# Kernel tuning notes

Hardware: AMD Instinct MI355X
Metric: run time of the kernel (lower is better)

## Reference

```python
import jax, jax.numpy as jnp
import numpy as np

D_MODEL = 2048
N_HEADS = 16
D_HEAD = 128
ROPE_BASE = 10000.0


def _rope(q, k, start_pos):
    # q, k: [B, H, S, Dh]; standard rotate-half RoPE
    S, Dh = q.shape[-2], q.shape[-1]
    inv_freq = 1.0 / (ROPE_BASE ** (jnp.arange(0, Dh, 2, dtype=jnp.float32) / Dh))  # [Dh/2]
    pos = jnp.arange(S, dtype=jnp.float32) + start_pos                              # [S]
    ang = pos[:, None] * inv_freq[None, :]                                          # [S, Dh/2]
    cos = jnp.concatenate([jnp.cos(ang), jnp.cos(ang)], axis=-1)[None, None]        # [1,1,S,Dh]
    sin = jnp.concatenate([jnp.sin(ang), jnp.sin(ang)], axis=-1)[None, None]

    def rot_half(t):
        t1, t2 = jnp.split(t, 2, axis=-1)
        return jnp.concatenate([-t2, t1], axis=-1)

    return q * cos + rot_half(q) * sin, k * cos + rot_half(k) * sin


def setup_inputs() -> dict:
    key = jax.random.key(0)
    k1, k2, k3 = jax.random.split(key, 3)
    B, S = 2, 2048
    scale_in = 1.0 / np.sqrt(D_MODEL)
    x = jax.random.normal(k1, (B, S, D_MODEL), dtype=jnp.float32)
    w_qkv = jax.random.normal(k2, (3 * D_MODEL, D_MODEL), dtype=jnp.float32) * scale_in
    w_out = jax.random.normal(k3, (D_MODEL, D_MODEL), dtype=jnp.float32) * scale_in
    return {"x": x, "w_qkv": w_qkv, "w_out": w_out, "start_pos": 0}


def reference(x, w_qkv, w_out, start_pos):
    B, S, _ = x.shape
    scale = 1.0 / np.sqrt(D_HEAD)
    qkv = jnp.einsum('bsd,ed->bse', x, w_qkv)                 # [B,S,3D]
    q, k, v = jnp.split(qkv, 3, axis=-1)
    # [B,S,D] -> [B,H,S,Dh]
    reshape = lambda t: t.reshape(B, S, N_HEADS, D_HEAD).transpose(0, 2, 1, 3)
    q, k, v = reshape(q), reshape(k), reshape(v)
    q, k = _rope(q, k, start_pos)
    scores = jnp.einsum('bhqd,bhkd->bhqk', q, k) * scale      # [B,H,S,S]
    if S > 1:
        causal = jnp.tril(jnp.ones((S, S), dtype=bool))
        scores = jnp.where(causal[None, None], scores, -jnp.inf)
    attn = jax.nn.softmax(scores, axis=-1)
    out = jnp.einsum('bhqk,bhkd->bhqd', attn, v)              # [B,H,S,Dh]
    out = out.transpose(0, 2, 1, 3).reshape(B, S, D_MODEL)
    return jnp.einsum('bsd,ed->bse', out, w_out)
```

## Files before the change

kernel.cpp:

```cpp
#include <hip/hip_runtime.h>

typedef unsigned short ushort;
typedef __attribute__((ext_vector_type(8))) short short8;
typedef __attribute__((ext_vector_type(4))) float f32x4;

#define NH 16
#define DH 128
#define SEQ 2048
#define DMODEL 2048
#define GK 2048

__device__ __forceinline__ ushort f2bf(float f) {
  union { float f; unsigned u; } v; v.f = f;
  unsigned u = v.u;
  unsigned r = (u + 0x7fffu + ((u >> 16) & 1u)) >> 16;
  return (ushort)r;
}
__device__ __forceinline__ float bf2f(ushort h) {
  union { unsigned u; float f; } v; v.u = ((unsigned)h) << 16; return v.f;
}

__device__ __forceinline__ void async16(const ushort* g, ushort* l) {
  __builtin_amdgcn_global_load_lds(
      (const __attribute__((address_space(1))) unsigned*)g,
      (__attribute__((address_space(3))) unsigned*)l, 16, 0, 0);
}

#define NX  2097152
#define NWQ 3145728
#define NWO 1048576
__global__ void cast3_kernel(const float* __restrict__ x, const float* __restrict__ wq,
                             const float* __restrict__ wo, ushort* __restrict__ xb,
                             ushort* __restrict__ wqb, ushort* __restrict__ wob) {
  int i = blockIdx.x * blockDim.x + threadIdx.x;
  int stride = gridDim.x * blockDim.x;
  for (; i < NX + NWQ + NWO; i += stride) {
    const float* s; ushort* d; int j;
    if (i < NX)            { s = x;  d = xb;  j = i; }
    else if (i < NX + NWQ) { s = wq; d = wqb; j = i - NX; }
    else                   { s = wo; d = wob; j = i - NX - NWQ; }
    float4 v = ((const float4*)s)[j];
    unsigned long long p = (unsigned long long)f2bf(v.x)
                         | ((unsigned long long)f2bf(v.y) << 16)
                         | ((unsigned long long)f2bf(v.z) << 32)
                         | ((unsigned long long)f2bf(v.w) << 48);
    ((unsigned long long*)d)[j] = p;
  }
}

template<int MODE, int NTK, int BN>
__global__ __launch_bounds__(512, 1)
void gemmk(const ushort* __restrict__ A, const ushort* __restrict__ B, int N,
           ushort* __restrict__ oq, ushort* __restrict__ ok, ushort* __restrict__ ov,
           float* __restrict__ of) {
  constexpr int NF = BN / 64;
  constexpr int WN = BN / 4;
  __shared__ ushort As[2][256 * 64];
  __shared__ ushort Bs[2][BN * 64];
  const int tid = threadIdx.x;
  const int lane = tid & 63;
  const int w = tid >> 6;
  const int wm = w >> 2, wn = w & 3;
  const int g = lane >> 4, l16 = lane & 15;
  const int m0 = blockIdx.y * 256;
  const int n0 = blockIdx.x * BN;
  const ushort* Ablk = A + (size_t)m0 * GK;
  const ushort* Bblk = B + (size_t)n0 * GK;

  const int r0 = tid >> 3, sl = tid & 7;
  const int gcol = ((sl * 16) ^ ((r0 & 7) << 4)) >> 1;
  const int ldsb = r0 * 64 + sl * 8;

  f32x4 acc[8][NF];
#pragma unroll
  for (int mf = 0; mf < 8; ++mf)
#pragma unroll
    for (int nf = 0; nf < NF; ++nf) acc[mf][nf] = (f32x4)0.f;

  short8 ra[4], rb[NF];
#pragma unroll
  for (int j = 0; j < 4; ++j)
    ra[j] = *(const short8*)(Ablk + (size_t)(j * 64 + r0) * GK + gcol);
#pragma unroll
  for (int j = 0; j < NF; ++j)
    rb[j] = *(const short8*)(Bblk + (size_t)(j * 64 + r0) * GK + gcol);
#pragma unroll
  for (int j = 0; j < 4; ++j) *(short8*)&As[0][j * 4096 + ldsb] = ra[j];
#pragma unroll
  for (int j = 0; j < NF; ++j) *(short8*)&Bs[0][j * 4096 + ldsb] = rb[j];
#pragma unroll
  for (int j = 0; j < 4; ++j)
    ra[j] = *(const short8*)(Ablk + (size_t)(j * 64 + r0) * GK + 64 + gcol);
#pragma unroll
  for (int j = 0; j < NF; ++j)
    rb[j] = *(const short8*)(Bblk + (size_t)(j * 64 + r0) * GK + 64 + gcol);
#pragma unroll
  for (int j = 0; j < 4; ++j) *(short8*)&As[1][j * 4096 + ldsb] = ra[j];
#pragma unroll
  for (int j = 0; j < NF; ++j) *(short8*)&Bs[1][j * 4096 + ldsb] = rb[j];
  __syncthreads();

  for (int t = 0; t < NTK; ++t) {
    const bool pre = (t + 2 < NTK);
    if (pre) {
      const int kt = (t + 2) * 64;
#pragma unroll
      for (int j = 0; j < 4; ++j)
        ra[j] = *(const short8*)(Ablk + (size_t)(j * 64 + r0) * GK + kt + gcol);
#pragma unroll
      for (int j = 0; j < NF; ++j)
        rb[j] = *(const short8*)(Bblk + (size_t)(j * 64 + r0) * GK + kt + gcol);
    }
    __builtin_amdgcn_sched_barrier(0);

    const ushort* cA = As[t & 1];
    const ushort* cB = Bs[t & 1];
    short8 bfr[NF][2];
#pragma unroll
    for (int nf = 0; nf < NF; ++nf) {
      int row = wn * WN + nf * 16 + l16;
#pragma unroll
      for (int ks = 0; ks < 2; ++ks)
        bfr[nf][ks] = *(const short8*)&cB[row * 64 + (((ks * 64 + g * 16) ^ ((l16 & 7) << 4)) >> 1)];
    }
#pragma unroll
    for (int p = 0; p < 4; ++p) {
      short8 af[2][2];
#pragma unroll
      for (int mi = 0; mi < 2; ++mi) {
        int row = wm * 128 + (2 * p + mi) * 16 + l16;
#pragma unroll
        for (int ks = 0; ks < 2; ++ks)
          af[mi][ks] = *(const short8*)&cA[row * 64 + (((ks * 64 + g * 16) ^ ((l16 & 7) << 4)) >> 1)];
      }
      __builtin_amdgcn_s_setprio(1);
#pragma unroll
      for (int mi = 0; mi < 2; ++mi)
#pragma unroll
        for (int nf = 0; nf < NF; ++nf)
#pragma unroll
          for (int ks = 0; ks < 2; ++ks)
            acc[2 * p + mi][nf] = __builtin_amdgcn_mfma_f32_16x16x32_bf16(
                af[mi][ks], bfr[nf][ks], acc[2 * p + mi][nf], 0, 0, 0);
      __builtin_amdgcn_s_setprio(0);
    }

    __syncthreads();
    if (pre) {
      ushort* nA = (ushort*)As[t & 1];
      ushort* nB = (ushort*)Bs[t & 1];
#pragma unroll
      for (int j = 0; j < 4; ++j) *(short8*)&nA[j * 4096 + ldsb] = ra[j];
#pragma unroll
      for (int j = 0; j < NF; ++j) *(short8*)&nB[j * 4096 + ldsb] = rb[j];
    }
  }

#pragma unroll
  for (int mf = 0; mf < 8; ++mf)
#pragma unroll
    for (int nf = 0; nf < NF; ++nf)
#pragma unroll
      for (int i = 0; i < 4; ++i) {
        int row = m0 + wm * 128 + mf * 16 + g * 4 + i;
        int col = n0 + wn * WN + nf * 16 + l16;
        float val = acc[mf][nf][i];
        if (MODE == 0) {
          int which = col >> 11;
          int r = col & 2047;
          int h = r >> 7, dh = r & 127;
          int b = row >> 11, s = row & 2047;
          size_t dst = ((size_t)(b * NH + h) * SEQ + s) * DH + dh;
          ushort* o = (which == 0) ? oq : (which == 1 ? ok : ov);
          o[dst] = f2bf(val);
        } else {
          of[(size_t)row * N + col] = val;
        }
      }
}

__global__ void rope_kernel(ushort* __restrict__ q, ushort* __restrict__ k,
                            const int* __restrict__ spp) {
  int id = blockIdx.x * blockDim.x + threadIdx.x;
  int j = id & 63;
  int s = (id >> 6) & (SEQ - 1);
  int bh = id >> 17;
  size_t base = ((size_t)bh * SEQ + s) * DH;
  float pos = (float)(s + spp[0]);
  float ang = pos * __expf(-(float)j * (9.210340371976184f / 64.f));
  float c = cosf(ang), sn = sinf(ang);
  float q1 = bf2f(q[base + j]), q2 = bf2f(q[base + 64 + j]);
  q[base + j]      = f2bf(q1 * c - q2 * sn);
  q[base + 64 + j] = f2bf(q2 * c + q1 * sn);
  float k1 = bf2f(k[base + j]), k2 = bf2f(k[base + 64 + j]);
  k[base + j]      = f2bf(k1 * c - k2 * sn);
  k[base + 64 + j] = f2bf(k2 * c + k1 * sn);
}

__global__ __launch_bounds__(256, 2)
void attn_kernel(const ushort* __restrict__ Q, const ushort* __restrict__ K,
                 const ushort* __restrict__ V, ushort* __restrict__ O) {
  __shared__ ushort Ks[2][64 * 128];
  __shared__ ushort Vt[2][128 * 72];
  __shared__ ushort Ps[4][16 * 72];
  const int tid = threadIdx.x;
  const int lane = tid & 63;
  const int w = tid >> 6;
  const int g = lane >> 4, l16 = lane & 15;
  const int h = blockIdx.y, b = blockIdx.z;
  const int bh = b * NH + h;
  const ushort* Qb = Q + (size_t)bh * SEQ * DH;
  const ushort* Kb = K + (size_t)bh * SEQ * DH;
  const ushort* Vb = V + (size_t)bh * SEQ * DH;
  const float scale2 = 0.08838834764831845f * 1.4426950408889634f;
  const float THR2   = 11.541560327111708f;

  const int vkv = (tid >> 3) * 2;
  const int vd0 = (tid & 7) * 16;
  const int vmask = (tid & 7) << 3;

  for (int pass = 0; pass < 2; ++pass) {
    const int qt = pass == 0 ? (31 - (int)blockIdx.x) : (int)blockIdx.x;
    const int q0 = qt * 64;
    const int nkt = qt + 1;

    short8 qf[4];
    {
      const ushort* qrow = Qb + (size_t)(q0 + w * 16 + l16) * DH;
#pragma unroll
      for (int ks = 0; ks < 4; ++ks) qf[ks] = *(const short8*)(qrow + ks * 32 + g * 8);
    }
    f32x4 oacc[8];
#pragma unroll
    for (int i = 0; i < 8; ++i) oacc[i] = (f32x4)0.f;
    float m_i[4], l_i[4];
#pragma unroll
    for (int i = 0; i < 4; ++i) { m_i[i] = -INFINITY; l_i[i] = 0.f; }

#pragma unroll
    for (int it = 0; it < 4; ++it) {
      int ci = it * 256 + tid;
      int row = ci >> 4;
      int cb = ((ci & 15) * 16) ^ ((row & 7) << 4);
      async16(Kb + (size_t)row * DH + (cb >> 1), &Ks[0][ci * 8]);
    }
    {
      short8 vr[4];
      vr[0] = *(const short8*)(Vb + (size_t)vkv * DH + vd0);
      vr[1] = *(const short8*)(Vb + (size_t)vkv * DH + vd0 + 8);
      vr[2] = *(const short8*)(Vb + (size_t)(vkv + 1) * DH + vd0);
      vr[3] = *(const short8*)(Vb + (size_t)(vkv + 1) * DH + vd0 + 8);
#pragma unroll
      for (int j = 0; j < 16; ++j) {
        int d = vd0 + j;
        const ushort* a = (const ushort*)&vr[j >> 3];
        const ushort* c = (const ushort*)&vr[2 + (j >> 3)];
        unsigned val = (unsigned)a[j & 7] | ((unsigned)c[j & 7] << 16);
        *(unsigned*)&Vt[0][d * 72 + (vkv ^ vmask)] = val;
      }
    }
    __syncthreads();

    int cur = 0;
    for (int t = 0; t < nkt; ++t) {
      const int k0 = t * 64;
      const int nxt = cur ^ 1;
      const bool pre = (t + 1 < nkt);
      short8 vr[4];
      if (pre) {
        const int kn = (t + 1) * 64;
#pragma unroll
        for (int it = 0; it < 4; ++it) {
          int ci = it * 256 + tid;
          int row = ci >> 4;
          int cb = ((ci & 15) * 16) ^ ((row & 7) << 4);
          async16(Kb + (size_t)(kn + row) * DH + (cb >> 1), &Ks[nxt][ci * 8]);
        }
        vr[0] = *(const short8*)(Vb + (size_t)(kn + vkv) * DH + vd0);
        vr[1] = *(const short8*)(Vb + (size_t)(kn + vkv) * DH + vd0 + 8);
        vr[2] = *(const short8*)(Vb + (size_t)(kn + vkv + 1) * DH + vd0);
        vr[3] = *(const short8*)(Vb + (size_t)(kn + vkv + 1) * DH + vd0 + 8);
      }

      f32x4 sacc[4];
#pragma unroll
      for (int nf = 0; nf < 4; ++nf) sacc[nf] = (f32x4)0.f;
      __builtin_amdgcn_s_setprio(1);
#pragma unroll
      for (int nf = 0; nf < 4; ++nf) {
        int row = nf * 16 + l16;
#pragma unroll
        for (int ks = 0; ks < 4; ++ks) {
          int cb = (ks * 64 + g * 16) ^ ((l16 & 7) << 4);
          short8 kf = *(const short8*)&Ks[cur][row * 128 + (cb >> 1)];
          sacc[nf] = __builtin_amdgcn_mfma_f32_16x16x32_bf16(qf[ks], kf, sacc[nf], 0, 0, 0);
        }
      }
      __builtin_amdgcn_s_setprio(0);

      float pv[4][4], mxr[4];
#pragma unroll
      for (int i = 0; i < 4; ++i)
#pragma unroll
        for (int nf = 0; nf < 4; ++nf) pv[i][nf] = sacc[nf][i] * scale2;
      if (t == nkt - 1) {
#pragma unroll
        for (int i = 0; i < 4; ++i) {
          int qrow = q0 + w * 16 + g * 4 + i;
#pragma unroll
          for (int nf = 0; nf < 4; ++nf)
            if (k0 + nf * 16 + l16 > qrow) pv[i][nf] = -INFINITY;
        }
      }
#pragma unroll
      for (int i = 0; i < 4; ++i) {
        float mx = fmaxf(fmaxf(pv[i][0], pv[i][1]), fmaxf(pv[i][2], pv[i][3]));
#pragma unroll
        for (int d = 1; d < 16; d <<= 1) mx = fmaxf(mx, __shfl_xor(mx, d, 64));
        mxr[i] = mx;
      }
      int need = 0;
#pragma unroll
      for (int i = 0; i < 4; ++i) need |= (mxr[i] > m_i[i] + THR2) ? 1 : 0;
      if (__any(need)) {
#pragma unroll
        for (int i = 0; i < 4; ++i) {
          float mnew = fmaxf(m_i[i], mxr[i]);
          float alpha = exp2f(m_i[i] - mnew);
          l_i[i] *= alpha;
          m_i[i] = mnew;
#pragma unroll
          for (int nf2 = 0; nf2 < 8; ++nf2) oacc[nf2][i] *= alpha;
        }
      }
#pragma unroll
      for (int i = 0; i < 4; ++i) {
        float p[4];
#pragma unroll
        for (int nf = 0; nf < 4; ++nf) p[nf] = exp2f(pv[i][nf] - m_i[i]);
        l_i[i] += (p[0] + p[1]) + (p[2] + p[3]);
#pragma unroll
        for (int nf = 0; nf < 4; ++nf)
          Ps[w][(g * 4 + i) * 72 + nf * 16 + l16] = f2bf(p[nf]);
      }
      __asm__ volatile("s_waitcnt lgkmcnt(0)" ::: "memory");
      __builtin_amdgcn_sched_barrier(0);

      __builtin_amdgcn_s_setprio(1);
#pragma unroll
      for (int kvh = 0; kvh < 2; ++kvh) {
        short8 pa = *(const short8*)&Ps[w][l16 * 72 + kvh * 32 + g * 8];
#pragma unroll
        for (int nf2 = 0; nf2 < 8; ++nf2) {
          int cb = (kvh * 32 + g * 8) ^ (nf2 * 8);
          short8 vf = *(const short8*)&Vt[cur][(nf2 * 16 + l16) * 72 + cb];
          oacc[nf2] = __builtin_amdgcn_mfma_f32_16x16x32_bf16(pa, vf, oacc[nf2], 0, 0, 0);
        }
      }
      __builtin_amdgcn_s_setprio(0);

      if (pre) {
#pragma unroll
        for (int j = 0; j < 16; ++j) {
          int d = vd0 + j;
          const ushort* a = (const ushort*)&vr[j >> 3];
          const ushort* c = (const ushort*)&vr[2 + (j >> 3)];
          unsigned val = (unsigned)a[j & 7] | ((unsigned)c[j & 7] << 16);
          *(unsigned*)&Vt[nxt][d * 72 + (vkv ^ vmask)] = val;
        }
      }
      __syncthreads();
      cur = nxt;
    }

#pragma unroll
    for (int i = 0; i < 4; ++i) {
      float sum = l_i[i];
#pragma unroll
      for (int d = 1; d < 16; d <<= 1) sum += __shfl_xor(sum, d, 64);
      float inv = 1.f / sum;
      int row = q0 + w * 16 + g * 4 + i;
      size_t obase = ((size_t)b * SEQ + row) * DMODEL + h * DH;
#pragma unroll
      for (int nf2 = 0; nf2 < 8; ++nf2)
        O[obase + nf2 * 16 + l16] = f2bf(oacc[nf2][i] * inv);
    }
  }
}

extern "C" void kernel_launch(void* const* d_in, const int* in_sizes, int n_in,
                              void* d_out, int out_size, void* d_ws, size_t ws_size,
                              hipStream_t stream) {
  const float* x    = (const float*)d_in[0];
  const float* wqkv = (const float*)d_in[1];
  const float* wout = (const float*)d_in[2];
  const int*   spp  = (const int*)d_in[3];
  float* out = (float*)d_out;

  ushort* ws = (ushort*)d_ws;
  ushort* xb  = ws;
  ushort* wqb = xb + 8388608;
  ushort* wob = wqb + 12582912;
  ushort* q   = wob + 4194304;
  ushort* k   = q + 8388608;
  ushort* v   = k + 8388608;
  ushort* ao  = v + 8388608;

  cast3_kernel<<<2048, 256, 0, stream>>>(x, wqkv, wout, xb, wqb, wob);

  gemmk<0, 32, 192><<<dim3(6144 / 192, 4096 / 256, 1), 512, 0, stream>>>(
      xb, wqb, 6144, q, k, v, nullptr);

  rope_kernel<<<4194304 / 256, 256, 0, stream>>>(q, k, spp);

  attn_kernel<<<dim3(16, NH, 2), 256, 0, stream>>>(q, k, v, ao);

  gemmk<1, 32, 128><<<dim3(2048 / 128, 4096 / 256, 1), 512, 0, stream>>>(
      ao, wob, 2048, nullptr, nullptr, nullptr, out);
}
```

Measured before the change: 261.4 us.

## Fuse fp32-to-bf16 cast into GEMM global loads, drop separate cast kernel

Removes the standalone cast kernel. Both GEMMs now read fp32 x and the weights directly and convert them to bf16 in registers with v_cvt_pk_bf16_f32 before storing to LDS. This saves a launch and a full write and re-read of bf16 copies. In exchange, each GEMM reads twice the bytes from global memory, and the weights are re-read by many blocks, so the GEMMs carry more traffic and use more registers.

```diff
diff --git a/kernel.cpp b/kernel.cpp
--- a/kernel.cpp
+++ b/kernel.cpp
@@ -20,37 +20,41 @@
   union { unsigned u; float f; } v; v.u = ((unsigned)h) << 16; return v.f;
 }
 
+__device__ __forceinline__ unsigned cvtpk(float lo, float hi) {
+  unsigned r;
+  asm("v_cvt_pk_bf16_f32 %0, %1, %2" : "=v"(r) : "v"(lo), "v"(hi));
+  return r;
+}
+
 __device__ __forceinline__ void async16(const ushort* g, ushort* l) {
   __builtin_amdgcn_global_load_lds(
       (const __attribute__((address_space(1))) unsigned*)g,
       (__attribute__((address_space(3))) unsigned*)l, 16, 0, 0);
 }
 
-#define NX  2097152
-#define NWQ 3145728
-#define NWO 1048576
-__global__ void cast3_kernel(const float* __restrict__ x, const float* __restrict__ wq,
-                             const float* __restrict__ wo, ushort* __restrict__ xb,
-                             ushort* __restrict__ wqb, ushort* __restrict__ wob) {
-  int i = blockIdx.x * blockDim.x + threadIdx.x;
-  int stride = gridDim.x * blockDim.x;
-  for (; i < NX + NWQ + NWO; i += stride) {
-    const float* s; ushort* d; int j;
-    if (i < NX)            { s = x;  d = xb;  j = i; }
-    else if (i < NX + NWQ) { s = wq; d = wqb; j = i - NX; }
-    else                   { s = wo; d = wob; j = i - NX - NWQ; }
-    float4 v = ((const float4*)s)[j];
-    unsigned long long p = (unsigned long long)f2bf(v.x)
-                         | ((unsigned long long)f2bf(v.y) << 16)
-                         | ((unsigned long long)f2bf(v.z) << 32)
-                         | ((unsigned long long)f2bf(v.w) << 48);
-    ((unsigned long long*)d)[j] = p;
+template<int F32> struct Chunk;
+template<> struct Chunk<0> {
+  short8 v;
+  __device__ __forceinline__ void load(const void* p) { v = *(const short8*)p; }
+  __device__ __forceinline__ short8 get() const { return v; }
+};
+template<> struct Chunk<1> {
+  f32x4 a, b;
+  __device__ __forceinline__ void load(const void* p) {
+    a = *(const f32x4*)p;
+    b = *(const f32x4*)((const float*)p + 4);
   }
-}
-
-template<int MODE, int NTK, int BN>
+  __device__ __forceinline__ short8 get() const {
+    union { unsigned u[4]; short8 s; } x;
+    x.u[0] = cvtpk(a[0], a[1]); x.u[1] = cvtpk(a[2], a[3]);
+    x.u[2] = cvtpk(b[0], b[1]); x.u[3] = cvtpk(b[2], b[3]);
+    return x.s;
+  }
+};
+
+template<int MODE, int NTK, int BN, int AF32, int BF32>
 __global__ __launch_bounds__(512, 1)
-void gemmk(const ushort* __restrict__ A, const ushort* __restrict__ B, int N,
+void gemmk(const void* __restrict__ A, const void* __restrict__ B, int N,
            ushort* __restrict__ oq, ushort* __restrict__ ok, ushort* __restrict__ ov,
            float* __restrict__ of) {
   constexpr int NF = BN / 64;
@@ -64,40 +68,44 @@
   const int g = lane >> 4, l16 = lane & 15;
   const int m0 = blockIdx.y * 256;
   const int n0 = blockIdx.x * BN;
-  const ushort* Ablk = A + (size_t)m0 * GK;
-  const ushort* Bblk = B + (size_t)n0 * GK;
 
   const int r0 = tid >> 3, sl = tid & 7;
   const int gcol = ((sl * 16) ^ ((r0 & 7) << 4)) >> 1;
   const int ldsb = r0 * 64 + sl * 8;
 
+  auto aAddr = [&](int row, int col) -> const void* {
+    return AF32 ? (const void*)((const float*)A + (size_t)(m0 + row) * GK + col)
+                : (const void*)((const ushort*)A + (size_t)(m0 + row) * GK + col);
+  };
+  auto bAddr = [&](int row, int col) -> const void* {
+    return BF32 ? (const void*)((const float*)B + (size_t)(n0 + row) * GK + col)
+                : (const void*)((const ushort*)B + (size_t)(n0 + row) * GK + col);
+  };
+
   f32x4 acc[8][NF];
 #pragma unroll
   for (int mf = 0; mf < 8; ++mf)
 #pragma unroll
     for (int nf = 0; nf < NF; ++nf) acc[mf][nf] = (f32x4)0.f;
 
-  short8 ra[4], rb[NF];
-#pragma unroll
-  for (int j = 0; j < 4; ++j)
-    ra[j] = *(const short8*)(Ablk + (size_t)(j * 64 + r0) * GK + gcol);
-#pragma unroll
-  for (int j = 0; j < NF; ++j)
-    rb[j] = *(const short8*)(Bblk + (size_t)(j * 64 + r0) * GK + gcol);
-#pragma unroll
-  for (int j = 0; j < 4; ++j) *(short8*)&As[0][j * 4096 + ldsb] = ra[j];
-#pragma unroll
-  for (int j = 0; j < NF; ++j) *(short8*)&Bs[0][j * 4096 + ldsb] = rb[j];
-#pragma unroll
-  for (int j = 0; j < 4; ++j)
-    ra[j] = *(const short8*)(Ablk + (size_t)(j * 64 + r0) * GK + 64 + gcol);
-#pragma unroll
-  for (int j = 0; j < NF; ++j)
-    rb[j] = *(const short8*)(Bblk + (size_t)(j * 64 + r0) * GK + 64 + gcol);
-#pragma unroll
-  for (int j = 0; j < 4; ++j) *(short8*)&As[1][j * 4096 + ldsb] = ra[j];
-#pragma unroll
-  for (int j = 0; j < NF; ++j) *(short8*)&Bs[1][j * 4096 + ldsb] = rb[j];
+  Chunk<AF32> ra[4];
+  Chunk<BF32> rb[NF];
+#pragma unroll
+  for (int j = 0; j < 4; ++j)  ra[j].load(aAddr(j * 64 + r0, gcol));
+#pragma unroll
+  for (int j = 0; j < NF; ++j) rb[j].load(bAddr(j * 64 + r0, gcol));
+#pragma unroll
+  for (int j = 0; j < 4; ++j)  *(short8*)&As[0][j * 4096 + ldsb] = ra[j].get();
+#pragma unroll
+  for (int j = 0; j < NF; ++j) *(short8*)&Bs[0][j * 4096 + ldsb] = rb[j].get();
+#pragma unroll
+  for (int j = 0; j < 4; ++j)  ra[j].load(aAddr(j * 64 + r0, 64 + gcol));
+#pragma unroll
+  for (int j = 0; j < NF; ++j) rb[j].load(bAddr(j * 64 + r0, 64 + gcol));
+#pragma unroll
+  for (int j = 0; j < 4; ++j)  *(short8*)&As[1][j * 4096 + ldsb] = ra[j].get();
+#pragma unroll
+  for (int j = 0; j < NF; ++j) *(short8*)&Bs[1][j * 4096 + ldsb] = rb[j].get();
   __syncthreads();
 
   for (int t = 0; t < NTK; ++t) {
@@ -105,11 +113,9 @@
     if (pre) {
       const int kt = (t + 2) * 64;
 #pragma unroll
-      for (int j = 0; j < 4; ++j)
-        ra[j] = *(const short8*)(Ablk + (size_t)(j * 64 + r0) * GK + kt + gcol);
-#pragma unroll
-      for (int j = 0; j < NF; ++j)
-        rb[j] = *(const short8*)(Bblk + (size_t)(j * 64 + r0) * GK + kt + gcol);
+      for (int j = 0; j < 4; ++j)  ra[j].load(aAddr(j * 64 + r0, kt + gcol));
+#pragma unroll
+      for (int j = 0; j < NF; ++j) rb[j].load(bAddr(j * 64 + r0, kt + gcol));
     }
     __builtin_amdgcn_sched_barrier(0);
 
@@ -150,9 +156,9 @@
       ushort* nA = (ushort*)As[t & 1];
       ushort* nB = (ushort*)Bs[t & 1];
 #pragma unroll
-      for (int j = 0; j < 4; ++j) *(short8*)&nA[j * 4096 + ldsb] = ra[j];
-#pragma unroll
-      for (int j = 0; j < NF; ++j) *(short8*)&nB[j * 4096 + ldsb] = rb[j];
+      for (int j = 0; j < 4; ++j)  *(short8*)&nA[j * 4096 + ldsb] = ra[j].get();
+#pragma unroll
+      for (int j = 0; j < NF; ++j) *(short8*)&nB[j * 4096 + ldsb] = rb[j].get();
     }
   }
 
@@ -398,23 +404,18 @@
   float* out = (float*)d_out;
 
   ushort* ws = (ushort*)d_ws;
-  ushort* xb  = ws;
-  ushort* wqb = xb + 8388608;
-  ushort* wob = wqb + 12582912;
-  ushort* q   = wob + 4194304;
+  ushort* q   = ws;
   ushort* k   = q + 8388608;
   ushort* v   = k + 8388608;
   ushort* ao  = v + 8388608;
 
-  cast3_kernel<<<2048, 256, 0, stream>>>(x, wqkv, wout, xb, wqb, wob);
-
-  gemmk<0, 32, 192><<<dim3(6144 / 192, 4096 / 256, 1), 512, 0, stream>>>(
-      xb, wqb, 6144, q, k, v, nullptr);
+  gemmk<0, 32, 192, 1, 1><<<dim3(6144 / 192, 4096 / 256, 1), 512, 0, stream>>>(
+      x, wqkv, 6144, q, k, v, nullptr);
 
   rope_kernel<<<4194304 / 256, 256, 0, stream>>>(q, k, spp);
 
   attn_kernel<<<dim3(16, NH, 2), 256, 0, stream>>>(q, k, v, ao);
 
-  gemmk<1, 32, 128><<<dim3(2048 / 128, 4096 / 256, 1), 512, 0, stream>>>(
-      ao, wob, 2048, nullptr, nullptr, nullptr, out);
-}
+  gemmk<1, 32, 128, 0, 1><<<dim3(2048 / 128, 4096 / 256, 1), 512, 0, stream>>>(
+      ao, wout, 2048, nullptr, nullptr, nullptr, out);
+}
```

Result: slower. 276.2 us (+5.7%).
